# Performance work log

Hardware: AMD Instinct MI355X
Metric: run time of the kernel (lower is better)

Reference implementation:

```python
import jax, jax.numpy as jnp
import numpy as np

EMBD_DIM = 1024
NUM_HEADS = 16
HEAD_DIM = EMBD_DIM // NUM_HEADS


def setup_inputs() -> dict:
    key = jax.random.key(0)
    ks = jax.random.split(key, 9)
    B, S, D = 2, 2048, EMBD_DIM
    scale = 1.0 / np.sqrt(D)
    return {
        "x": jax.random.normal(ks[0], (B, S, D), dtype=jnp.float32),
        "wq": jax.random.normal(ks[1], (D, D), dtype=jnp.float32) * scale,
        "bq": jnp.zeros((D,), dtype=jnp.float32),
        "wk": jax.random.normal(ks[2], (D, D), dtype=jnp.float32) * scale,
        "bk": jnp.zeros((D,), dtype=jnp.float32),
        "wv": jax.random.normal(ks[3], (D, D), dtype=jnp.float32) * scale,
        "bv": jnp.zeros((D,), dtype=jnp.float32),
        "wo": jax.random.normal(ks[4], (D, D), dtype=jnp.float32) * scale,
        "bo": jnp.zeros((D,), dtype=jnp.float32),
    }


def reference(x, wq, bq, wk, bk, wv, bv, wo, bo):
    B, S, D = x.shape
    H, hd = NUM_HEADS, HEAD_DIM
    # projections: weights stored as (in, out) so y = x @ w + b
    q = (x @ wq + bq).reshape(B, S, H, hd).transpose(0, 2, 1, 3)  # [B,H,S,hd]
    k = (x @ wk + bk).reshape(B, S, H, hd).transpose(0, 2, 1, 3)
    v = (x @ wv + bv).reshape(B, S, H, hd).transpose(0, 2, 1, 3)
    scores = jnp.einsum("bhqd,bhkd->bhqk", q, k) / jnp.sqrt(jnp.float32(hd))
    causal = jnp.tril(jnp.ones((S, S), dtype=bool))  # [S,S]
    neg = jnp.finfo(scores.dtype).min
    scores = jnp.where(causal[None, None, :, :], scores, neg)
    attn = jax.nn.softmax(scores, axis=-1)
    out = jnp.einsum("bhqk,bhkd->bhqd", attn, v)  # [B,H,S,hd]
    out = out.transpose(0, 2, 1, 3).reshape(B, S, D)
    return out @ wo + bo
```

## Files before the change

kernel.cpp:

```cpp
#include <hip/hip_runtime.h>
#include <math.h>

#define S_LEN 2048
#define BATCH 2
#define DMODEL 1024
#define NHEADS 16
#define MROWS 4096

typedef short bf8 __attribute__((ext_vector_type(8)));
typedef short bf4 __attribute__((ext_vector_type(4)));
typedef float f32x4 __attribute__((ext_vector_type(4)));
typedef unsigned short u16;

static __device__ inline u16 f2bf(float f) {
    union { float f; unsigned u; } v; v.f = f;
    unsigned r = v.u + 0x7fffu + ((v.u >> 16) & 1u);
    return (u16)(r >> 16);
}

static __device__ inline void load16(const void* g, void* l) {
    __builtin_amdgcn_global_load_lds(
        (const __attribute__((address_space(1))) unsigned int*)g,
        (__attribute__((address_space(3))) unsigned int*)l, 16, 0, 0);
}

__global__ __launch_bounds__(256) void prep_kernel(
    const float* __restrict__ x, u16* __restrict__ xb,
    const float* __restrict__ W0, const float* __restrict__ W1,
    const float* __restrict__ W2, const float* __restrict__ W3,
    u16* __restrict__ wT) {
    const int bx = blockIdx.x, t = threadIdx.x;
    if (bx < 2048) {
        int i = bx * 256 + t;
        const float4* p = (const float4*)x + (size_t)i * 2;
        float4 a = p[0], b = p[1];
        u16 tmp[8] = {f2bf(a.x), f2bf(a.y), f2bf(a.z), f2bf(a.w),
                      f2bf(b.x), f2bf(b.y), f2bf(b.z), f2bf(b.w)};
        ((uint4*)xb)[i] = *(uint4*)tmp;
        return;
    }
    __shared__ u16 Ls[64][65];
    const int id = bx - 2048;
    const int z = id >> 8, rem = id & 255;
    const int n0 = (rem & 15) * 64, k0 = (rem >> 4) * 64;
    const float* W = z == 0 ? W0 : z == 1 ? W1 : z == 2 ? W2 : W3;
    u16* Wt = wT + (size_t)z * 1024 * 1024;
    const int r = t >> 2, c4 = (t & 3) * 16;
    const float* p = W + (size_t)(k0 + r) * 1024 + n0 + c4;
#pragma unroll
    for (int i = 0; i < 16; i += 4) {
        float4 v = *(const float4*)(p + i);
        Ls[r][c4 + i + 0] = f2bf(v.x);
        Ls[r][c4 + i + 1] = f2bf(v.y);
        Ls[r][c4 + i + 2] = f2bf(v.z);
        Ls[r][c4 + i + 3] = f2bf(v.w);
    }
    __syncthreads();
    u16 tmp[16];
#pragma unroll
    for (int i = 0; i < 16; i++) tmp[i] = Ls[c4 + i][r];
    uint4* q = (uint4*)(Wt + (size_t)(n0 + r) * 1024 + k0 + c4);
    q[0] = *(uint4*)tmp;
    q[1] = *(uint4*)(tmp + 8);
}

template <int MODE>
__global__ __launch_bounds__(256) void gemm_mfma(
    const u16* __restrict__ A, const u16* __restrict__ Bt,
    const float* __restrict__ bqp, const float* __restrict__ bkp,
    const float* __restrict__ bvp,
    u16* __restrict__ qout, u16* __restrict__ kout, u16* __restrict__ vtout,
    float* __restrict__ fout, float qscale) {
    constexpr int TM = (MODE == 1) ? 64 : 128;
    constexpr int MI = (MODE == 1) ? 2 : 4;
    constexpr int ADMA = (MODE == 1) ? 2 : 4;
    __shared__ __align__(16) u16 As[TM * 64];
    __shared__ __align__(16) u16 Bs[128 * 64];

    const int t = threadIdx.x, lane = t & 63, w = t >> 6;
    const int quad = lane >> 4, l16 = lane & 15;
    const int row0 = blockIdx.y * TM, col0 = blockIdx.x * 128;
    const int fq = (MODE == 1) ? w * 32 : (w & 1) * 64;
    const int xq = (MODE == 1) ? 0 : (w >> 1) * 64;
    const int K = DMODEL;

    const int lrow = lane >> 3;
    const int koff = ((lane & 7) ^ lrow) * 8;
    const int abase = (MODE == 1) ? w * 16 : w * 32;
    const u16* ag = A + (size_t)(row0 + abase + lrow) * K + koff;
    const u16* bg = Bt + (size_t)(col0 + w * 32 + lrow) * K + koff;
    u16* lA = As + abase * 64;
    u16* lB = Bs + (w * 32) * 64;
    const int swz = l16 & 7;

    f32x4 acc[MI][4] = {};

    for (int k0 = 0; k0 < K; k0 += 64) {
#pragma unroll
        for (int d = 0; d < ADMA; d++)
            load16(ag + (size_t)d * 8 * K + k0, lA + d * 512);
#pragma unroll
        for (int d = 0; d < 4; d++)
            load16(bg + (size_t)d * 8 * K + k0, lB + d * 512);
        __syncthreads();
#pragma unroll
        for (int kc = 0; kc < 2; kc++) {
            bf8 xf[4], wf[MI];
#pragma unroll
            for (int ni = 0; ni < 4; ni++)
                xf[ni] = *(const bf8*)&As[(xq + ni * 16 + l16) * 64 +
                                          ((kc * 4 + quad) ^ swz) * 8];
#pragma unroll
            for (int mi = 0; mi < MI; mi++)
                wf[mi] = *(const bf8*)&Bs[(fq + mi * 16 + l16) * 64 +
                                          ((kc * 4 + quad) ^ swz) * 8];
#pragma unroll
            for (int mi = 0; mi < MI; mi++)
#pragma unroll
                for (int ni = 0; ni < 4; ni++)
                    acc[mi][ni] = __builtin_amdgcn_mfma_f32_16x16x32_bf16(
                        wf[mi], xf[ni], acc[mi][ni], 0, 0, 0);
        }
        __syncthreads();
    }

    const int sect = (col0 + fq) >> 10;
#pragma unroll
    for (int mi = 0; mi < MI; mi++) {
        const int featb = col0 + fq + mi * 16 + quad * 4;
        float b4[4];
#pragma unroll
        for (int reg = 0; reg < 4; reg++)
            b4[reg] = (MODE == 1 ? bqp : (sect == 0 ? bqp : sect == 1 ? bkp : bvp))
                          [(featb + reg) & 1023];
#pragma unroll
        for (int ni = 0; ni < 4; ni++) {
            const int xrow = row0 + xq + ni * 16 + l16;
            if (MODE == 1) {
                float4 o;
                o.x = acc[mi][ni][0] + b4[0];
                o.y = acc[mi][ni][1] + b4[1];
                o.z = acc[mi][ni][2] + b4[2];
                o.w = acc[mi][ni][3] + b4[3];
                *(float4*)(fout + (size_t)xrow * 1024 + featb) = o;
            } else {
                const int cf = featb & 1023;
                if (sect == 0) {
                    u16 t4[4];
#pragma unroll
                    for (int reg = 0; reg < 4; reg++)
                        t4[reg] = f2bf((acc[mi][ni][reg] + b4[reg]) * qscale);
                    *(uint2*)(qout + (size_t)xrow * 1024 + cf) = *(uint2*)t4;
                } else if (sect == 1) {
                    u16 t4[4];
#pragma unroll
                    for (int reg = 0; reg < 4; reg++)
                        t4[reg] = f2bf(acc[mi][ni][reg] + b4[reg]);
                    *(uint2*)(kout + (size_t)xrow * 1024 + cf) = *(uint2*)t4;
                } else {
#pragma unroll
                    for (int reg = 0; reg < 4; reg++)
                        vtout[((size_t)(xrow >> 11) * 1024 + cf + reg) * S_LEN +
                              (xrow & 2047)] = f2bf(acc[mi][ni][reg] + b4[reg]);
                }
            }
        }
    }
}

__global__ __launch_bounds__(256) void attn_kernel(const u16* __restrict__ Qg,
                                                   const u16* __restrict__ Kg,
                                                   const u16* __restrict__ Vt,
                                                   u16* __restrict__ Og) {
    __shared__ __align__(16) u16 Ks[2][64][32];
    __shared__ __align__(16) u16 Vs[2][64][32];

    const int t = threadIdx.x, lane = t & 63, w = t >> 6;
    const int quad = lane >> 4, l16 = lane & 15;
    const int pi = blockIdx.y;
    const int bh = blockIdx.x, b = bh >> 4, h = bh & 15;
    const size_t base = (size_t)b * S_LEN * DMODEL + h * 64;
    const size_t vbase = ((size_t)b * 1024 + h * 64) * S_LEN;
    const int sr = t >> 2, sc = (t & 3) * 16;
    const int pl = sc >> 5;
    const int g0 = (sc >> 3) & 3;
    const int ss = (sr >> 1) & 3;
    const int swz = (l16 >> 1) & 3;

    const u16* kp = Kg + base + (size_t)sr * DMODEL + sc;
    const u16* vp = Vt + vbase + (size_t)sr * S_LEN + sc;
    uint4 k0r = *(const uint4*)kp, k1r = *(const uint4*)(kp + 8);
    uint4 v0r = *(const uint4*)vp, v1r = *(const uint4*)(vp + 8);

#pragma unroll
    for (int seg = 0; seg < 2; seg++) {
        const int qt = seg == 0 ? pi : 31 - pi;
        const int niter = qt + 1;
        const int q0 = qt * 64;

        bf8 aq[2];
#pragma unroll
        for (int c = 0; c < 2; c++)
            aq[c] = *(const bf8*)(Qg + base +
                (size_t)(q0 + w * 16 + l16) * DMODEL + c * 32 + quad * 8);

        float lsum = 0.f;
        f32x4 oT[4] = {};

        for (int kt = 0; kt < niter; kt++) {
            __syncthreads();
            *(uint4*)&Ks[pl][sr][(g0 ^ ss) * 8] = k0r;
            *(uint4*)&Ks[pl][sr][((g0 + 1) ^ ss) * 8] = k1r;
            *(uint4*)&Vs[pl][sr][(g0 ^ ss) * 8] = v0r;
            *(uint4*)&Vs[pl][sr][((g0 + 1) ^ ss) * 8] = v1r;
            __syncthreads();
            if (!(seg == 1 && kt + 1 == niter)) {
                int nt = (kt + 1 < niter) ? kt + 1 : 0;
                size_t ok = (size_t)nt * 64 * DMODEL;
                int ov = nt * 64;
                k0r = *(const uint4*)(kp + ok); k1r = *(const uint4*)(kp + ok + 8);
                v0r = *(const uint4*)(vp + ov); v1r = *(const uint4*)(vp + ov + 8);
            }

            f32x4 scv[4] = {};
#pragma unroll
            for (int c = 0; c < 2; c++)
#pragma unroll
                for (int ns = 0; ns < 4; ns++) {
                    bf8 ak = *(const bf8*)&Ks[c][ns * 16 + l16][(quad ^ swz) * 8];
                    scv[ns] = __builtin_amdgcn_mfma_f32_16x16x32_bf16(
                        ak, aq[c], scv[ns], 0, 0, 0);
                }

            const bool diag = (kt == qt);
            const int ql = w * 16 + l16;
#pragma unroll
            for (int ns = 0; ns < 4; ns++) {
                float p[4];
#pragma unroll
                for (int r = 0; r < 4; r++) {
                    int key = ns * 16 + quad * 4 + r;
                    p[r] = (diag && key > ql) ? 0.f
                                              : __builtin_amdgcn_exp2f(scv[ns][r]);
                    lsum += p[r];
                }
                union { unsigned u[2]; bf4 v; } pk;
                pk.u[0] = (__float_as_uint(p[0]) >> 16) |
                          (__float_as_uint(p[1]) & 0xffff0000u);
                pk.u[1] = (__float_as_uint(p[2]) >> 16) |
                          (__float_as_uint(p[3]) & 0xffff0000u);
#pragma unroll
                for (int ds = 0; ds < 4; ds++) {
                    bf4 av = *(const bf4*)&Vs[ns >> 1][ds * 16 + l16]
                        [((((ns & 1) * 2 + (quad >> 1)) ^ swz) * 8) + (quad & 1) * 4];
                    oT[ds] = __builtin_amdgcn_mfma_f32_16x16x16bf16_1k(
                        av, pk.v, oT[ds], 0, 0, 0);
                }
            }
        }

        float l = lsum;
        l += __shfl_xor(l, 16, 64);
        l += __shfl_xor(l, 32, 64);
        const float inv = 1.f / l;
        const int qq = q0 + w * 16 + l16;
#pragma unroll
        for (int ds = 0; ds < 4; ds++) {
            u16 t4[4];
#pragma unroll
            for (int r = 0; r < 4; r++) t4[r] = f2bf(oT[ds][r] * inv);
            *(uint2*)(Og + base + (size_t)qq * DMODEL + ds * 16 + quad * 4) =
                *(uint2*)t4;
        }
    }
}

extern "C" void kernel_launch(void* const* d_in, const int* in_sizes, int n_in,
                              void* d_out, int out_size, void* d_ws, size_t ws_size,
                              hipStream_t stream) {
    const float* x  = (const float*)d_in[0];
    const float* wq = (const float*)d_in[1];
    const float* bq = (const float*)d_in[2];
    const float* wk = (const float*)d_in[3];
    const float* bk = (const float*)d_in[4];
    const float* wv = (const float*)d_in[5];
    const float* bv = (const float*)d_in[6];
    const float* wo = (const float*)d_in[7];
    const float* bo = (const float*)d_in[8];
    float* out = (float*)d_out;

    const size_t E = (size_t)MROWS * DMODEL;
    u16* xb  = (u16*)d_out;
    u16* vt  = xb + E;
    u16* wT  = (u16*)d_ws;
    u16* woT = wT + 3145728;
    u16* qb  = wT + 4194304;
    u16* kb  = qb + E;
    u16* ob  = kb + E;

    dim3 blk(256);
    prep_kernel<<<3072, blk, 0, stream>>>(x, xb, wq, wk, wv, wo, wT);

    gemm_mfma<0><<<dim3(24, 32), blk, 0, stream>>>(
        xb, wT, bq, bk, bv, qb, kb, vt, nullptr, 0.18033688011112042f);

    dim3 agrid(BATCH * NHEADS, 16);
    attn_kernel<<<agrid, blk, 0, stream>>>(qb, kb, vt, ob);

    gemm_mfma<1><<<dim3(8, 64), blk, 0, stream>>>(
        ob, woT, bo, nullptr, nullptr, nullptr, nullptr, nullptr, out, 1.0f);
}
```

Baseline: 192.4 us.

## Double-buffer GEMM LDS tiles and use 64-row tiles for QKV projection

The GEMM kernel now keeps two LDS buffers and issues the global-to-LDS loads for the next K-slice before computing on the current one, so memory transfer overlaps MFMA work and one barrier per iteration is dropped. The QKV projection also switches from 128x128 tiles to the 64x128 tile used by the output projection, doubling its grid. This adds LDS use and more blocks, with lower per-block reuse of the B tile, in exchange for better latency hiding and occupancy.

```diff
diff --git a/kernel.cpp b/kernel.cpp
--- a/kernel.cpp
+++ b/kernel.cpp
@@ -71,63 +71,70 @@
     const float* __restrict__ bvp,
     u16* __restrict__ qout, u16* __restrict__ kout, u16* __restrict__ vtout,
     float* __restrict__ fout, float qscale) {
-    constexpr int TM = (MODE == 1) ? 64 : 128;
-    constexpr int MI = (MODE == 1) ? 2 : 4;
-    constexpr int ADMA = (MODE == 1) ? 2 : 4;
-    __shared__ __align__(16) u16 As[TM * 64];
-    __shared__ __align__(16) u16 Bs[128 * 64];
+    __shared__ __align__(16) u16 As[2][64 * 64];
+    __shared__ __align__(16) u16 Bs[2][128 * 64];
 
     const int t = threadIdx.x, lane = t & 63, w = t >> 6;
     const int quad = lane >> 4, l16 = lane & 15;
-    const int row0 = blockIdx.y * TM, col0 = blockIdx.x * 128;
-    const int fq = (MODE == 1) ? w * 32 : (w & 1) * 64;
-    const int xq = (MODE == 1) ? 0 : (w >> 1) * 64;
+    const int row0 = blockIdx.y * 64, col0 = blockIdx.x * 128;
     const int K = DMODEL;
 
     const int lrow = lane >> 3;
     const int koff = ((lane & 7) ^ lrow) * 8;
-    const int abase = (MODE == 1) ? w * 16 : w * 32;
-    const u16* ag = A + (size_t)(row0 + abase + lrow) * K + koff;
+    const u16* ag = A + (size_t)(row0 + w * 16 + lrow) * K + koff;
     const u16* bg = Bt + (size_t)(col0 + w * 32 + lrow) * K + koff;
-    u16* lA = As + abase * 64;
-    u16* lB = Bs + (w * 32) * 64;
     const int swz = l16 & 7;
 
-    f32x4 acc[MI][4] = {};
-
-    for (int k0 = 0; k0 < K; k0 += 64) {
-#pragma unroll
-        for (int d = 0; d < ADMA; d++)
-            load16(ag + (size_t)d * 8 * K + k0, lA + d * 512);
+    f32x4 acc[2][4] = {};
+
+    {
+        u16* lA = As[0] + (w * 16) * 64;
+        u16* lB = Bs[0] + (w * 32) * 64;
+        load16(ag, lA);
+        load16(ag + (size_t)8 * K, lA + 512);
 #pragma unroll
         for (int d = 0; d < 4; d++)
-            load16(bg + (size_t)d * 8 * K + k0, lB + d * 512);
+            load16(bg + (size_t)d * 8 * K, lB + d * 512);
+    }
+
+#pragma unroll 2
+    for (int it = 0; it < 16; it++) {
+        const int buf = it & 1;
         __syncthreads();
+        if (it + 1 < 16) {
+            const int k0 = (it + 1) * 64;
+            u16* lA = As[buf ^ 1] + (w * 16) * 64;
+            u16* lB = Bs[buf ^ 1] + (w * 32) * 64;
+            load16(ag + k0, lA);
+            load16(ag + (size_t)8 * K + k0, lA + 512);
+#pragma unroll
+            for (int d = 0; d < 4; d++)
+                load16(bg + (size_t)d * 8 * K + k0, lB + d * 512);
+        }
 #pragma unroll
         for (int kc = 0; kc < 2; kc++) {
-            bf8 xf[4], wf[MI];
+            bf8 xf[4], wf[2];
 #pragma unroll
             for (int ni = 0; ni < 4; ni++)
-                xf[ni] = *(const bf8*)&As[(xq + ni * 16 + l16) * 64 +
-                                          ((kc * 4 + quad) ^ swz) * 8];
-#pragma unroll
-            for (int mi = 0; mi < MI; mi++)
-                wf[mi] = *(const bf8*)&Bs[(fq + mi * 16 + l16) * 64 +
-                                          ((kc * 4 + quad) ^ swz) * 8];
-#pragma unroll
-            for (int mi = 0; mi < MI; mi++)
+                xf[ni] = *(const bf8*)&As[buf][(ni * 16 + l16) * 64 +
+                                              ((kc * 4 + quad) ^ swz) * 8];
+#pragma unroll
+            for (int mi = 0; mi < 2; mi++)
+                wf[mi] = *(const bf8*)&Bs[buf][(w * 32 + mi * 16 + l16) * 64 +
+                                              ((kc * 4 + quad) ^ swz) * 8];
+#pragma unroll
+            for (int mi = 0; mi < 2; mi++)
 #pragma unroll
                 for (int ni = 0; ni < 4; ni++)
                     acc[mi][ni] = __builtin_amdgcn_mfma_f32_16x16x32_bf16(
                         wf[mi], xf[ni], acc[mi][ni], 0, 0, 0);
         }
-        __syncthreads();
-    }
-
-    const int sect = (col0 + fq) >> 10;
-#pragma unroll
-    for (int mi = 0; mi < MI; mi++) {
-        const int featb = col0 + fq + mi * 16 + quad * 4;
+    }
+
+    const int sect = (col0 + w * 32) >> 10;
+#pragma unroll
+    for (int mi = 0; mi < 2; mi++) {
+        const int featb = col0 + w * 32 + mi * 16 + quad * 4;
         float b4[4];
 #pragma unroll
         for (int reg = 0; reg < 4; reg++)
@@ -135,7 +142,7 @@
                           [(featb + reg) & 1023];
 #pragma unroll
         for (int ni = 0; ni < 4; ni++) {
-            const int xrow = row0 + xq + ni * 16 + l16;
+            const int xrow = row0 + ni * 16 + l16;
             if (MODE == 1) {
                 float4 o;
                 o.x = acc[mi][ni][0] + b4[0];
@@ -301,7 +308,7 @@
     dim3 blk(256);
     prep_kernel<<<3072, blk, 0, stream>>>(x, xb, wq, wk, wv, wo, wT);
 
-    gemm_mfma<0><<<dim3(24, 32), blk, 0, stream>>>(
+    gemm_mfma<0><<<dim3(24, 64), blk, 0, stream>>>(
         xb, wT, bq, bk, bv, qb, kb, vt, nullptr, 0.18033688011112042f);
 
     dim3 agrid(BATCH * NHEADS, 16);
```

Result: no change. 192.0 us (-0.2%).
